# Optimization experiments

Hardware: AMD Instinct MI355X
Metric: run time of the kernel (lower is better)

Reference implementation:

```python
import jax, jax.numpy as jnp
import numpy as np

D_MODEL = 768
N_HEADS = 12
D_KEYS = 64
D_LLM = 4096
D_INNER = N_HEADS * D_KEYS  # 768


def setup_inputs() -> dict:
    key = jax.random.key(0)
    ks = jax.random.split(key, 12)
    inp = {
        "target_embedding": jax.random.normal(ks[0], (8, 1024, D_MODEL), dtype=jnp.float32),
        "source_embedding": jax.random.normal(ks[1], (1000, D_LLM), dtype=jnp.float32),
        "value_embedding": jax.random.normal(ks[2], (1000, D_LLM), dtype=jnp.float32),
        # Linear params stored as [in, out] (y = x @ W + b)
        "Wq": jax.random.normal(ks[3], (D_MODEL, D_INNER), dtype=jnp.float32) * 0.02,
        "bq": jnp.zeros((D_INNER,), dtype=jnp.float32),
        "Wk": jax.random.normal(ks[4], (D_LLM, D_INNER), dtype=jnp.float32) * 0.02,
        "bk": jnp.zeros((D_INNER,), dtype=jnp.float32),
        "Wv": jax.random.normal(ks[5], (D_LLM, D_INNER), dtype=jnp.float32) * 0.02,
        "bv": jnp.zeros((D_INNER,), dtype=jnp.float32),
        "Wo": jax.random.normal(ks[6], (D_INNER, D_LLM), dtype=jnp.float32) * 0.02,
        "bo": jnp.zeros((D_LLM,), dtype=jnp.float32),
    }
    return inp


def reference(target_embedding, source_embedding, value_embedding,
              Wq, bq, Wk, bk, Wv, bv, Wo, bo):
    B, L, _ = target_embedding.shape
    S, _ = source_embedding.shape
    H, E = N_HEADS, D_KEYS
    # projections
    q = (target_embedding @ Wq + bq).reshape(B, L, H, E)  # [B,L,H,E]
    k = (source_embedding @ Wk + bk).reshape(S, H, E)     # [S,H,E] broadcast over batch
    v = (value_embedding @ Wv + bv).reshape(S, H, E)      # [S,H,E]
    scale = 1.0 / np.sqrt(E).astype(np.float32)
    scores = jnp.einsum('blhe,she->bhls', q, k) * scale   # [B,H,L,S]
    A = jax.nn.softmax(scores, axis=-1)                   # dropout is identity at eval
    out = jnp.einsum('bhls,she->blhe', A, v).reshape(B, L, H * E)
    return out @ Wo + bo                                  # [B,L,d_llm]
```

## Files before the change

### kernel.cpp

```cpp
#include <hip/hip_runtime.h>
#include <cstdint>
#include <type_traits>


typedef unsigned short u16;
typedef __attribute__((ext_vector_type(8))) short bf16x8;
typedef __attribute__((ext_vector_type(4))) float f32x4;
typedef __attribute__((ext_vector_type(16))) float f32x16;
typedef __attribute__((ext_vector_type(4))) float fvec4;
typedef __attribute__((ext_vector_type(4))) unsigned short u16x4;
typedef __attribute__((ext_vector_type(4))) unsigned int u32x4;
typedef __attribute__((ext_vector_type(2))) unsigned int u32x2;

using gld_src_t = const __attribute__((address_space(1))) void*;
using gld_dst_t = __attribute__((address_space(3))) void*;

static __device__ __forceinline__ u16 bf16_rne(float f) {
  uint32_t u = __builtin_bit_cast(uint32_t, f);
  u += 0x7fffu + ((u >> 16) & 1u);
  return (u16)(u >> 16);
}

static __device__ __forceinline__ float exp2_fast(float x) {
  float r; asm("v_exp_f32 %0, %1" : "=v"(r) : "v"(x)); return r;
}

static __device__ __forceinline__ uint32_t pk_bf16(float a, float b) {
  return (uint32_t)bf16_rne(a) | ((uint32_t)bf16_rne(b) << 16);
}

__global__ void convert_pad_bf16(const float* __restrict__ in, u16* __restrict__ out,
                                 int validR, int C, long n4) {
  long stride = (long)gridDim.x * blockDim.x;
  for (long i = (long)blockIdx.x * blockDim.x + threadIdx.x; i < n4; i += stride) {
    long e = i << 2;
    int r = (int)(e / C);
    u16x4 o;
    if (r < validR) {
      fvec4 v = *(const fvec4*)(in + e);
      o[0] = bf16_rne(v[0]); o[1] = bf16_rne(v[1]);
      o[2] = bf16_rne(v[2]); o[3] = bf16_rne(v[3]);
    } else {
      o[0] = 0; o[1] = 0; o[2] = 0; o[3] = 0;
    }
    *(u16x4*)(out + e) = o;
  }
}

template <bool F32IN>
__global__ void transpose_to_bf16(const void* __restrict__ inv, u16* __restrict__ out,
                                  int R, int C) {
  __shared__ u16 tile[32][33];
  int bc = blockIdx.x * 32, br = blockIdx.y * 32;
  int tx = threadIdx.x & 31, ty = threadIdx.x >> 5;
#pragma unroll
  for (int i = 0; i < 4; ++i) {
    int r = br + ty + i * 8, c = bc + tx;
    u16 bits = 0;
    if (r < R && c < C) {
      if constexpr (F32IN) bits = bf16_rne(((const float*)inv)[(size_t)r * C + c]);
      else                 bits = ((const u16*)inv)[(size_t)r * C + c];
    }
    tile[ty + i * 8][tx] = bits;
  }
  __syncthreads();
#pragma unroll
  for (int i = 0; i < 4; ++i) {
    int orow = bc + ty + i * 8, oc = br + tx;
    if (orow < C && oc < R) out[(size_t)orow * R + oc] = tile[tx][ty + i * 8];
  }
}

template <typename CT>
__global__ __launch_bounds__(256) void gemm_bt_128(
    const u16* __restrict__ A0, const u16* __restrict__ A1,
    const u16* __restrict__ B0, const u16* __restrict__ B1,
    const float* __restrict__ bias0, const float* __restrict__ bias1,
    CT* __restrict__ C0, CT* __restrict__ C1,
    int M, int N, int K, float escale) {
  const u16* A = blockIdx.z ? A1 : A0;
  const u16* B = blockIdx.z ? B1 : B0;
  const float* bias = blockIdx.z ? bias1 : bias0;
  CT* C = blockIdx.z ? C1 : C0;
  (void)M;

  __shared__ u16 As[128 * 32];
  __shared__ u16 Bs[128 * 32];

  const int tid = threadIdx.x;
  const int w = tid >> 6, lane = tid & 63;
  const int lr = lane & 15, lg = lane >> 4;
  const int bm = blockIdx.y * 128, bn = blockIdx.x * 128;
  const int wr = (w >> 1) * 64, wc = (w & 1) * 64;

  f32x4 acc[4][4] = {};

  const int nk = K >> 5;
  for (int kt = 0; kt < nk; ++kt) {
#pragma unroll
    for (int j = 0; j < 2; ++j) {
      int cb = j * 256 + w * 64;
      int c = cb + lane;
      const u16* gA = A + (size_t)(bm + (c >> 2)) * K + (size_t)kt * 32 + (c & 3) * 8;
      __builtin_amdgcn_global_load_lds((gld_src_t)(const void*)gA,
                                       (gld_dst_t)(As + (size_t)cb * 8), 16, 0, 0);
      const u16* gB = B + (size_t)(bn + (c >> 2)) * K + (size_t)kt * 32 + (c & 3) * 8;
      __builtin_amdgcn_global_load_lds((gld_src_t)(const void*)gB,
                                       (gld_dst_t)(Bs + (size_t)cb * 8), 16, 0, 0);
    }
    __syncthreads();

    bf16x8 af[4], bfr[4];
#pragma unroll
    for (int m = 0; m < 4; ++m)
      af[m] = *(const bf16x8*)(As + (wr + m * 16 + lr) * 32 + lg * 8);
#pragma unroll
    for (int n = 0; n < 4; ++n)
      bfr[n] = *(const bf16x8*)(Bs + (wc + n * 16 + lr) * 32 + lg * 8);
#pragma unroll
    for (int m = 0; m < 4; ++m)
#pragma unroll
      for (int n = 0; n < 4; ++n)
        acc[m][n] = __builtin_amdgcn_mfma_f32_16x16x32_bf16(af[m], bfr[n], acc[m][n], 0, 0, 0);
    __syncthreads();
  }

#pragma unroll
  for (int n = 0; n < 4; ++n) {
    int col = bn + wc + n * 16 + lr;
    float bv = bias[col];
#pragma unroll
    for (int m = 0; m < 4; ++m) {
      int row0 = bm + wr + m * 16 + lg * 4;
#pragma unroll
      for (int r = 0; r < 4; ++r) {
        float v = (acc[m][n][r] + bv) * escale;
        if constexpr (std::is_same<CT, u16>::value)
          C[(size_t)(row0 + r) * N + col] = bf16_rne(v);
        else
          C[(size_t)(row0 + r) * N + col] = v;
      }
    }
  }
}

__global__ __launch_bounds__(256) void gemm_kv_splitk(
    const u16* __restrict__ Sb, const u16* __restrict__ Vbi,
    const u16* __restrict__ WkT, const u16* __restrict__ WvT,
    float* __restrict__ part) {
  const int z = blockIdx.z;
  const u16* A = (z >> 2) ? Vbi : Sb;
  const u16* B = (z >> 2) ? WvT : WkT;
  float* C = part + (size_t)z * (1024 * 768);
  const int kofs = (z & 3) * 1024;

  __shared__ u16 As[128 * 32];
  __shared__ u16 Bs[128 * 32];
  const int tid = threadIdx.x, w = tid >> 6, lane = tid & 63;
  const int lr = lane & 15, lg = lane >> 4;
  const int bm = blockIdx.y * 128, bn = blockIdx.x * 128;
  const int wr = (w >> 1) * 64, wc = (w & 1) * 64;
  f32x4 acc[4][4] = {};

  for (int kt = 0; kt < 32; ++kt) {
#pragma unroll
    for (int j = 0; j < 2; ++j) {
      int cb = j * 256 + w * 64;
      int c = cb + lane;
      const u16* gA = A + (size_t)(bm + (c >> 2)) * 4096 + kofs + kt * 32 + (c & 3) * 8;
      __builtin_amdgcn_global_load_lds((gld_src_t)(const void*)gA,
                                       (gld_dst_t)(As + (size_t)cb * 8), 16, 0, 0);
      const u16* gB = B + (size_t)(bn + (c >> 2)) * 4096 + kofs + kt * 32 + (c & 3) * 8;
      __builtin_amdgcn_global_load_lds((gld_src_t)(const void*)gB,
                                       (gld_dst_t)(Bs + (size_t)cb * 8), 16, 0, 0);
    }
    __syncthreads();
    bf16x8 af[4], bfr[4];
#pragma unroll
    for (int m = 0; m < 4; ++m)
      af[m] = *(const bf16x8*)(As + (wr + m * 16 + lr) * 32 + lg * 8);
#pragma unroll
    for (int n = 0; n < 4; ++n)
      bfr[n] = *(const bf16x8*)(Bs + (wc + n * 16 + lr) * 32 + lg * 8);
#pragma unroll
    for (int m = 0; m < 4; ++m)
#pragma unroll
      for (int n = 0; n < 4; ++n)
        acc[m][n] = __builtin_amdgcn_mfma_f32_16x16x32_bf16(af[m], bfr[n], acc[m][n], 0, 0, 0);
    __syncthreads();
  }
#pragma unroll
  for (int n = 0; n < 4; ++n) {
    int col = bn + wc + n * 16 + lr;
#pragma unroll
    for (int m = 0; m < 4; ++m) {
      int row0 = bm + wr + m * 16 + lg * 4;
#pragma unroll
      for (int r = 0; r < 4; ++r)
        C[(size_t)(row0 + r) * 768 + col] = acc[m][n][r];
    }
  }
}

__global__ __launch_bounds__(256) void kv_reduce(const float* __restrict__ part,
                                                 const float* __restrict__ bk,
                                                 const float* __restrict__ bv,
                                                 u16* __restrict__ Kp, u16* __restrict__ Vp) {
  const int mat = blockIdx.y;
  const long e = ((long)blockIdx.x * 256 + threadIdx.x) * 4;
  const float* p0 = part + (size_t)mat * 4 * 786432 + e;
  fvec4 s = *(const fvec4*)p0;
  s += *(const fvec4*)(p0 + 786432);
  s += *(const fvec4*)(p0 + 2 * 786432);
  s += *(const fvec4*)(p0 + 3 * 786432);
  const float* bias = mat ? bv : bk;
  int col = (int)(e % 768);
  fvec4 bb = *(const fvec4*)(bias + col);
  s += bb;
  u16x4 o;
  o[0] = bf16_rne(s[0]); o[1] = bf16_rne(s[1]); o[2] = bf16_rne(s[2]); o[3] = bf16_rne(s[3]);
  u16* dst = mat ? Vp : Kp;
  *(u16x4*)(dst + e) = o;
}

__global__ __launch_bounds__(256, 3) void attn_flash(
    const u16* __restrict__ Q,
    const u16* __restrict__ Kb,
    const u16* __restrict__ VT,
    u16* __restrict__ O) {
  constexpr int DM = 768, SPAD = 1024;
  __shared__ u16 Ks[2][64 * 64];
  __shared__ u16 VTs[2][64 * 64];

  const int tid = threadIdx.x, w = tid >> 6, lane = tid & 63;
  const int q5 = lane & 31, hi = lane >> 5, l7 = lane & 7;
  const int h = blockIdx.y;
  const int qrow = blockIdx.x * 128 + w * 32 + q5;

  bf16x8 qf[4];
#pragma unroll
  for (int dstep = 0; dstep < 4; ++dstep)
    qf[dstep] = *(const bf16x8*)(Q + (size_t)qrow * DM + h * 64 + dstep * 16 + hi * 8);

  auto STAGE = [&](int ch, int buf) {
#pragma unroll
    for (int it = 0; it < 2; ++it) {
      int slot = it * 256 + w * 64 + lane;
      int row = slot >> 3;
      int cg = (slot & 7) ^ (row & 7);
      __builtin_amdgcn_global_load_lds(
          (gld_src_t)(const void*)(Kb + (size_t)(ch * 64 + row) * DM + h * 64 + cg * 8),
          (gld_dst_t)(&Ks[buf][(size_t)(it * 256 + w * 64) * 8]), 16, 0, 0);
      __builtin_amdgcn_global_load_lds(
          (gld_src_t)(const void*)(VT + (size_t)(h * 64 + row) * SPAD + ch * 64 + cg * 8),
          (gld_dst_t)(&VTs[buf][(size_t)(it * 256 + w * 64) * 8]), 16, 0, 0);
    }
  };

  STAGE(0, 0);
  __syncthreads();

  float m_run = -3.0e38f, l_part = 0.0f;
  f32x16 oa0 = {}, oa1 = {};

  for (int ch = 0; ch < 16; ++ch) {
    const int cur = ch & 1;
    if (ch < 15) STAGE(ch + 1, cur ^ 1);

    const char* kbase = (const char*)&Ks[cur][0];
    const char* vbase = (const char*)&VTs[cur][0];

    f32x16 sc0 = {}, sc1 = {};
#pragma unroll
    for (int dstep = 0; dstep < 4; ++dstep) {
      const int colb = (dstep * 32 + hi * 16);
      bf16x8 kf0 = *(const bf16x8*)(kbase + (size_t)q5 * 128 + (colb ^ (l7 << 4)));
      bf16x8 kf1 = *(const bf16x8*)(kbase + (size_t)(32 + q5) * 128 + (colb ^ (l7 << 4)));
      sc0 = __builtin_amdgcn_mfma_f32_32x32x16_bf16(kf0, qf[dstep], sc0, 0, 0, 0);
      sc1 = __builtin_amdgcn_mfma_f32_32x32x16_bf16(kf1, qf[dstep], sc1, 0, 0, 0);
    }
    if (ch == 15) {
#pragma unroll
      for (int r = 4; r < 16; ++r) sc1[r] = -3.0e38f;
    }

    float mi = sc0[0];
#pragma unroll
    for (int r = 1; r < 16; ++r) mi = fmaxf(mi, sc0[r]);
#pragma unroll
    for (int r = 0; r < 16; ++r) mi = fmaxf(mi, sc1[r]);
    float cm = fmaxf(mi, __shfl_xor(mi, 32, 64));

    if (__any(cm > m_run + 8.0f)) {
      float mn = fmaxf(m_run, cm);
      float fsc = exp2_fast(m_run - mn);
      m_run = mn;
      l_part *= fsc;
#pragma unroll
      for (int r = 0; r < 16; ++r) { oa0[r] *= fsc; oa1[r] *= fsc; }
    }

#pragma unroll
    for (int r = 0; r < 16; ++r) {
      float p0 = exp2_fast(sc0[r] - m_run); l_part += p0; sc0[r] = p0;
      float p1 = exp2_fast(sc1[r] - m_run); l_part += p1; sc1[r] = p1;
    }

#pragma unroll
    for (int st = 0; st < 2; ++st) {
#pragma unroll
      for (int ks = 0; ks < 2; ++ks) {
        float pv0, pv1, pv2, pv3, pv4, pv5, pv6, pv7;
        if (st == 0) {
          if (ks == 0) { pv0=sc0[0];pv1=sc0[1];pv2=sc0[2];pv3=sc0[3];pv4=sc0[4];pv5=sc0[5];pv6=sc0[6];pv7=sc0[7]; }
          else         { pv0=sc0[8];pv1=sc0[9];pv2=sc0[10];pv3=sc0[11];pv4=sc0[12];pv5=sc0[13];pv6=sc0[14];pv7=sc0[15]; }
        } else {
          if (ks == 0) { pv0=sc1[0];pv1=sc1[1];pv2=sc1[2];pv3=sc1[3];pv4=sc1[4];pv5=sc1[5];pv6=sc1[6];pv7=sc1[7]; }
          else         { pv0=sc1[8];pv1=sc1[9];pv2=sc1[10];pv3=sc1[11];pv4=sc1[12];pv5=sc1[13];pv6=sc1[14];pv7=sc1[15]; }
        }
        uint32_t a = pk_bf16(pv0, pv1), b = pk_bf16(pv2, pv3);
        uint32_t c = pk_bf16(pv4, pv5), d = pk_bf16(pv6, pv7);
        uint32_t sa = (uint32_t)__shfl_xor((int)a, 32, 64);
        uint32_t sb = (uint32_t)__shfl_xor((int)b, 32, 64);
        uint32_t sc_ = (uint32_t)__shfl_xor((int)c, 32, 64);
        uint32_t sd = (uint32_t)__shfl_xor((int)d, 32, 64);
        u32x4 jw;
        jw[0] = hi ? sc_ : a;
        jw[1] = hi ? sd  : b;
        jw[2] = hi ? c   : sa;
        jw[3] = hi ? d   : sb;
        bf16x8 pB = __builtin_bit_cast(bf16x8, jw);
        const int colb = (st * 64 + ks * 32 + hi * 16);
#pragma unroll
        for (int dt = 0; dt < 2; ++dt) {
          bf16x8 vtf = *(const bf16x8*)(vbase + (size_t)(dt * 32 + q5) * 128 + (colb ^ (l7 << 4)));
          if (dt == 0) oa0 = __builtin_amdgcn_mfma_f32_32x32x16_bf16(vtf, pB, oa0, 0, 0, 0);
          else         oa1 = __builtin_amdgcn_mfma_f32_32x32x16_bf16(vtf, pB, oa1, 0, 0, 0);
        }
      }
    }
    __syncthreads();
  }

  float ool = 1.0f / (l_part + __shfl_xor(l_part, 32, 64));
  u16* obase = O + (size_t)qrow * DM + h * 64;
#pragma unroll
  for (int dt = 0; dt < 2; ++dt) {
#pragma unroll
    for (int g = 0; g < 4; ++g) {
      float v0, v1, v2, v3;
      if (dt == 0) { v0 = oa0[4*g]; v1 = oa0[4*g+1]; v2 = oa0[4*g+2]; v3 = oa0[4*g+3]; }
      else         { v0 = oa1[4*g]; v1 = oa1[4*g+1]; v2 = oa1[4*g+2]; v3 = oa1[4*g+3]; }
      u32x2 st2;
      st2[0] = pk_bf16(v0 * ool, v1 * ool);
      st2[1] = pk_bf16(v2 * ool, v3 * ool);
      *(u32x2*)(obase + dt * 32 + g * 8 + hi * 4) = st2;
    }
  }
}

extern "C" void kernel_launch(void* const* d_in, const int* in_sizes, int n_in,
                              void* d_out, int out_size, void* d_ws, size_t ws_size,
                              hipStream_t stream) {
  (void)in_sizes; (void)n_in; (void)out_size; (void)ws_size;
  const float* target = (const float*)d_in[0];
  const float* source = (const float*)d_in[1];
  const float* value  = (const float*)d_in[2];
  const float* Wq = (const float*)d_in[3];
  const float* bq = (const float*)d_in[4];
  const float* Wk = (const float*)d_in[5];
  const float* bk = (const float*)d_in[6];
  const float* Wv = (const float*)d_in[7];
  const float* bv = (const float*)d_in[8];
  const float* Wo = (const float*)d_in[9];
  const float* bo = (const float*)d_in[10];
  float* out = (float*)d_out;

  char* ws = (char*)d_ws;
  size_t off = 0;
  auto carve = [&](size_t bytes) { void* p = ws + off; off += (bytes + 255) & ~(size_t)255; return p; };
  u16* Xb  = (u16*)carve(8192ull * 768 * 2);
  u16* Sb  = (u16*)carve(1024ull * 4096 * 2);
  u16* Vbi = (u16*)carve(1024ull * 4096 * 2);
  u16* WqT = (u16*)carve(768ull * 768 * 2);
  u16* WkT = (u16*)carve(768ull * 4096 * 2);
  u16* WvT = (u16*)carve(768ull * 4096 * 2);
  u16* WoT = (u16*)carve(4096ull * 768 * 2);
  u16* Qb  = (u16*)carve(8192ull * 768 * 2);
  u16* Kp  = (u16*)carve(1024ull * 768 * 2);
  u16* Vp  = (u16*)carve(1024ull * 768 * 2);
  u16* VTp = (u16*)carve(768ull * 1024 * 2);
  u16* Ob  = (u16*)carve(8192ull * 768 * 2);

  const float SCL = 0.18033688011112042f;

  convert_pad_bf16<<<2048, 256, 0, stream>>>(target, Xb, 8192, 768, (8192ll * 768) / 4);
  convert_pad_bf16<<<2048, 256, 0, stream>>>(source, Sb, 1000, 4096, (1024ll * 4096) / 4);
  convert_pad_bf16<<<2048, 256, 0, stream>>>(value,  Vbi, 1000, 4096, (1024ll * 4096) / 4);
  transpose_to_bf16<true><<<dim3(24, 24),  256, 0, stream>>>(Wq, WqT, 768, 768);
  transpose_to_bf16<true><<<dim3(24, 128), 256, 0, stream>>>(Wk, WkT, 4096, 768);
  transpose_to_bf16<true><<<dim3(24, 128), 256, 0, stream>>>(Wv, WvT, 4096, 768);
  transpose_to_bf16<true><<<dim3(128, 24), 256, 0, stream>>>(Wo, WoT, 768, 4096);

  gemm_kv_splitk<<<dim3(6, 8, 8), 256, 0, stream>>>(Sb, Vbi, WkT, WvT, out);
  kv_reduce<<<dim3(768, 2), 256, 0, stream>>>(out, bk, bv, Kp, Vp);
  transpose_to_bf16<false><<<dim3(24, 32), 256, 0, stream>>>(Vp, VTp, 1024, 768);

  gemm_bt_128<u16><<<dim3(6, 64, 1), 256, 0, stream>>>(Xb, Xb, WqT, WqT, bq, bq, Qb, Qb,
                                                       8192, 768, 768, SCL);

  attn_flash<<<dim3(64, 12), 256, 0, stream>>>(Qb, Kp, VTp, Ob);

  gemm_bt_128<float><<<dim3(32, 64, 1), 256, 0, stream>>>(Ob, Ob, WoT, WoT, bo, bo, out, out,
                                                          8192, 4096, 768, 1.0f);
}
```

Baseline: 232.7 us.

## Use 256x256 double-buffered tile GEMM for output projection

Replaces the 128x128 tile GEMM for the final O@Wo projection with a new 512-thread kernel that computes 256x256 tiles. It uses K-step 64, direct global-to-LDS loads into double buffers, an XOR-swizzled LDS layout, and a grouped block-index swizzle. The aim is more operand reuse per loaded byte and overlap of the next tile's loads with current MFMA work. The trade-off is 128KB of LDS per block and higher register pressure, and only 512 blocks are launched.

Result: faster. 225.8 us (-3.0%).

```diff
diff --git a/kernel.cpp b/kernel.cpp
--- a/kernel.cpp
+++ b/kernel.cpp
@@ -140,6 +140,104 @@
         else
           C[(size_t)(row0 + r) * N + col] = v;
       }
+    }
+  }
+}
+
+__global__ __launch_bounds__(512, 2) void gemm_bt_256(
+    const u16* __restrict__ A, const u16* __restrict__ B,
+    const float* __restrict__ bias, float* __restrict__ C,
+    int M, int N, int K) {
+  __shared__ u16 As[2][256 * 64];
+  __shared__ u16 Bs[2][256 * 64];
+  (void)M;
+
+  const int tid = threadIdx.x, lane = tid & 63, w = tid >> 6;
+  const int lr = lane & 15, lg = lane >> 4;
+  const int wr = w >> 2, wcol = w & 3;
+
+  const int nbx = N >> 8;
+  const int bid = blockIdx.y * gridDim.x + blockIdx.x;
+  const int cpx = (gridDim.x * gridDim.y) >> 3;
+  const int swz = (bid & 7) * cpx + (bid >> 3);
+  const int bm = (swz / nbx) * 256, bn = (swz % nbx) * 256;
+
+  f32x4 acc[8][4] = {};
+
+  auto STAGE = [&](int t, int buf) {
+#pragma unroll
+    for (int h = 0; h < 2; ++h)
+#pragma unroll
+      for (int it = 0; it < 2; ++it) {
+        const int s = it * 512 + tid;
+        const int r = s >> 3;
+        const int cg = (s & 7) ^ (r & 7);
+        const int row = h * 128 + r;
+        const int ldsb = h * 16384 + (it * 512 + w * 64) * 16;
+        __builtin_amdgcn_global_load_lds(
+            (gld_src_t)(const void*)(A + (size_t)(bm + row) * K + t * 64 + cg * 8),
+            (gld_dst_t)((char*)&As[buf][0] + ldsb), 16, 0, 0);
+        __builtin_amdgcn_global_load_lds(
+            (gld_src_t)(const void*)(B + (size_t)(bn + row) * K + t * 64 + cg * 8),
+            (gld_dst_t)((char*)&Bs[buf][0] + ldsb), 16, 0, 0);
+      }
+  };
+
+  auto LDF = [&](const u16* base, int R, int CB) {
+    return *(const bf16x8*)((const char*)base + (size_t)R * 128 + (CB ^ ((R & 7) << 4)));
+  };
+
+  STAGE(0, 0);
+  __syncthreads();
+
+  const int nk = K >> 6;
+  for (int t = 0; t < nk; ++t) {
+    const int cur = t & 1;
+    if (t + 1 < nk) STAGE(t + 1, cur ^ 1);
+    const u16* as = &As[cur][0];
+    const u16* bs = &Bs[cur][0];
+
+    bf16x8 bfrag[4][2];
+#pragma unroll
+    for (int nf = 0; nf < 4; ++nf)
+#pragma unroll
+      for (int kk = 0; kk < 2; ++kk)
+        bfrag[nf][kk] = LDF(bs, wcol * 64 + nf * 16 + lr, kk * 64 + lg * 16);
+
+#pragma unroll
+    for (int q = 0; q < 4; ++q) {
+      bf16x8 af[2][2];
+#pragma unroll
+      for (int m2 = 0; m2 < 2; ++m2)
+#pragma unroll
+        for (int kk = 0; kk < 2; ++kk)
+          af[m2][kk] = LDF(as, wr * 128 + (q * 2 + m2) * 16 + lr, kk * 64 + lg * 16);
+      __builtin_amdgcn_s_setprio(1);
+#pragma unroll
+      for (int m2 = 0; m2 < 2; ++m2)
+#pragma unroll
+        for (int kk = 0; kk < 2; ++kk)
+#pragma unroll
+          for (int nf = 0; nf < 4; ++nf)
+            acc[q * 2 + m2][nf] = __builtin_amdgcn_mfma_f32_16x16x32_bf16(
+                af[m2][kk], bfrag[nf][kk], acc[q * 2 + m2][nf], 0, 0, 0);
+      __builtin_amdgcn_s_setprio(0);
+    }
+    __syncthreads();
+  }
+
+  float bv[4];
+#pragma unroll
+  for (int nf = 0; nf < 4; ++nf) bv[nf] = bias[bn + wcol * 64 + nf * 16 + lr];
+#pragma unroll
+  for (int mf = 0; mf < 8; ++mf) {
+    const int row0 = bm + wr * 128 + mf * 16 + lg * 4;
+#pragma unroll
+    for (int nf = 0; nf < 4; ++nf) {
+      const int col = bn + wcol * 64 + nf * 16 + lr;
+#pragma unroll
+      for (int r = 0; r < 4; ++r)
+        C[(size_t)(row0 + r) * N + col] = acc[mf][nf][r] + bv[nf];
     }
   }
 }
@@ -411,6 +509,5 @@
 
   attn_flash<<<dim3(64, 12), 256, 0, stream>>>(Qb, Kp, VTp, Ob);
 
-  gemm_bt_128<float><<<dim3(32, 64, 1), 256, 0, stream>>>(Ob, Ob, WoT, WoT, bo, bo, out, out,
-                                                          8192, 4096, 768, 1.0f);
-}
+  gemm_bt_256<<<dim3(16, 32), 512, 0, stream>>>(Ob, WoT, bo, out, 8192, 4096, 768);
+}
```
